# Kernel optimization log

Measured on AMD Instinct MI355X. Metric: run time of the kernel, lower is better.

Reference implementation:

```python
import jax, jax.numpy as jnp
import numpy as np

NUM_HEADS = 4
NUM_GROUPS = 32
EPS = 1e-5


def setup_inputs() -> dict:
    key = jax.random.key(0)
    ks = jax.random.split(key, 5)
    c = 256
    x = jax.random.normal(ks[0], (2, c, 64, 64), dtype=jnp.float32)
    gn_w = jnp.ones((c,), dtype=jnp.float32)
    gn_b = jnp.zeros((c,), dtype=jnp.float32)
    qkv_w = jax.random.normal(ks[1], (3 * c, c), dtype=jnp.float32) * 0.02
    qkv_b = jax.random.normal(ks[2], (3 * c,), dtype=jnp.float32) * 0.02
    proj_w = jax.random.normal(ks[3], (c, c), dtype=jnp.float32) * 0.02
    proj_b = jnp.zeros((c,), dtype=jnp.float32)
    return {"x": x, "gn_w": gn_w, "gn_b": gn_b, "qkv_w": qkv_w,
            "qkv_b": qkv_b, "proj_w": proj_w, "proj_b": proj_b}


def reference(x, gn_w, gn_b, qkv_w, qkv_b, proj_w, proj_b):
    b, c, H, W = x.shape
    T = H * W
    xf = x.reshape(b, c, T)

    # GroupNorm(32, c): stats over (channels-in-group, T)
    xg = xf.reshape(b, NUM_GROUPS, c // NUM_GROUPS, T)
    mu = jnp.mean(xg, axis=(2, 3), keepdims=True)
    var = jnp.var(xg, axis=(2, 3), keepdims=True)
    xn = ((xg - mu) * jax.lax.rsqrt(var + EPS)).reshape(b, c, T)
    xn = xn * gn_w[None, :, None] + gn_b[None, :, None]

    # 1x1 conv1d == channel matmul: [3c, c] @ [b, c, T]
    qkv = jnp.einsum('oc,bct->bot', qkv_w, xn) + qkv_b[None, :, None]

    nh = NUM_HEADS
    ch = c // nh
    # reshape exactly as torch: (b, 3c, T) -> (b*nh, 3c//nh, T), split along dim 1
    qkv = qkv.reshape(b * nh, 3 * ch, T)
    q, k, v = jnp.split(qkv, 3, axis=1)

    scale = 1.0 / ch ** 0.25
    w = jnp.einsum('bct,bcs->bts', q * scale, k * scale)  # [b*nh, T, T]
    w = jax.nn.softmax(w, axis=-1)
    h = jnp.einsum('bts,bcs->bct', w, v)  # [b*nh, ch, T]

    h = h.reshape(b, c, T)
    h = jnp.einsum('oc,bct->bot', proj_w, h) + proj_b[None, :, None]
    return (xf + h).reshape(b, c, H, W)
```

## Files before the change

### kernel.cpp

```cpp
#include <hip/hip_runtime.h>
#include <hip/hip_bf16.h>

typedef float  f32x4  __attribute__((ext_vector_type(4)));
typedef float  f32x16 __attribute__((ext_vector_type(16)));
typedef short  s16x8  __attribute__((ext_vector_type(8)));
typedef __bf16 b16x8  __attribute__((ext_vector_type(8)));
typedef unsigned int u32x4 __attribute__((ext_vector_type(4)));

#define DI static __device__ __forceinline__

constexpr int BATCH = 2;
constexpr int C     = 256;
constexpr int T     = 4096;
constexpr int NG    = 32;
constexpr int CPG   = 8;
constexpr int NH    = 4;
constexpr int CH    = 64;

constexpr size_t STATS_OFF = 0;
constexpr size_t QKVW_OFF  = 4096;
constexpr size_t PROJW_OFF = QKVW_OFF + 393216;
constexpr size_t XNT_OFF   = PROJW_OFF + 131072;
constexpr size_t Q_OFF     = XNT_OFF + 4194304;
constexpr size_t K_OFF     = Q_OFF + 4194304;
constexpr size_t V_OFF     = K_OFF + 4194304;
constexpr size_t H_OFF     = V_OFF + 4194304;

template <typename V>
DI auto mfma_try(V a, V b, f32x4 c, int)
    -> decltype(__builtin_amdgcn_mfma_f32_16x16x32_bf16(a, b, c, 0, 0, 0)) {
  return __builtin_amdgcn_mfma_f32_16x16x32_bf16(a, b, c, 0, 0, 0);
}
template <typename V>
DI f32x4 mfma_try(V a, V b, f32x4 c, long) {
  return __builtin_amdgcn_mfma_f32_16x16x32_bf16(
      __builtin_bit_cast(b16x8, a), __builtin_bit_cast(b16x8, b), c, 0, 0, 0);
}
DI f32x4 MFMA(s16x8 a, s16x8 b, f32x4 c) { return mfma_try(a, b, c, 0); }

template <typename V>
DI auto mfma32_try(V a, V b, f32x16 c, int)
    -> decltype(__builtin_amdgcn_mfma_f32_32x32x16_bf16(a, b, c, 0, 0, 0)) {
  return __builtin_amdgcn_mfma_f32_32x32x16_bf16(a, b, c, 0, 0, 0);
}
template <typename V>
DI f32x16 mfma32_try(V a, V b, f32x16 c, long) {
  return __builtin_amdgcn_mfma_f32_32x32x16_bf16(
      __builtin_bit_cast(b16x8, a), __builtin_bit_cast(b16x8, b), c, 0, 0, 0);
}
DI f32x16 MFMA32(s16x8 a, s16x8 b, f32x16 c) { return mfma32_try(a, b, c, 0); }

DI unsigned short f2b(float f) {
  return __builtin_bit_cast(unsigned short, __float2bfloat16(f));
}
DI s16x8 ld8(const unsigned short* p) { return *(const s16x8*)p; }

DI float exp2f_(float x) {
#if __has_builtin(__builtin_amdgcn_exp2f)
  return __builtin_amdgcn_exp2f(x);
#else
  return exp2f(x);
#endif
}

DI unsigned cvtpk(float lo, float hi) {
  unsigned r;
  asm("v_cvt_pk_bf16_f32 %0, %1, %2" : "=v"(r) : "v"(lo), "v"(hi));
  return r;
}

DI void swap32(unsigned& a, unsigned& b) {
#if __has_builtin(__builtin_amdgcn_permlane32_swap)
  auto r = __builtin_amdgcn_permlane32_swap((int)a, (int)b, false, false);
  a = (unsigned)r[0];
  b = (unsigned)r[1];
#else
  unsigned as = (unsigned)__shfl_xor((int)a, 32);
  unsigned bs = (unsigned)__shfl_xor((int)b, 32);
  if (threadIdx.x & 32) a = bs; else b = as;
#endif
}

DI void stage16(const void* g, void* l) {
  __builtin_amdgcn_global_load_lds((__attribute__((address_space(1))) const void*)g,
                                   (__attribute__((address_space(3))) void*)l, 16, 0, 0);
}

DI float vsum16(f32x16 v) {
  float p0 = (v[0] + v[1]) + (v[2] + v[3]);
  float p1 = (v[4] + v[5]) + (v[6] + v[7]);
  float p2 = (v[8] + v[9]) + (v[10] + v[11]);
  float p3 = (v[12] + v[13]) + (v[14] + v[15]);
  return (p0 + p1) + (p2 + p3);
}

constexpr float SC2 = 0.18033688011f;

__global__ __launch_bounds__(256) void k_prep(const float* __restrict__ x,
                                              float2* __restrict__ part,
                                              const float* __restrict__ qkvw,
                                              const float* __restrict__ projw,
                                              uint2* __restrict__ qwb,
                                              uint2* __restrict__ pwb) {
  int blk = blockIdx.x;
  if (blk < 256) {
    const float4* base = (const float4*)(x + (size_t)blk * 8192);
    float s = 0.f, ss = 0.f;
    for (int i = threadIdx.x; i < 2048; i += 256) {
      float4 v = base[i];
      s  += v.x + v.y + v.z + v.w;
      ss += v.x * v.x + v.y * v.y + v.z * v.z + v.w * v.w;
    }
#pragma unroll
    for (int off = 32; off > 0; off >>= 1) {
      s  += __shfl_down(s, off);
      ss += __shfl_down(ss, off);
    }
    __shared__ float sm[4], sm2[4];
    int wid = threadIdx.x >> 6;
    if ((threadIdx.x & 63) == 0) { sm[wid] = s; sm2[wid] = ss; }
    __syncthreads();
    if (threadIdx.x == 0)
      part[blk] = make_float2(sm[0] + sm[1] + sm[2] + sm[3], sm2[0] + sm2[1] + sm2[2] + sm2[3]);
  } else {
    int i = (blk - 256) * 256 + threadIdx.x;
    if (i < 3 * C * C / 4) {
      float4 v = ((const float4*)qkvw)[i];
      qwb[i] = make_uint2(cvtpk(v.x, v.y), cvtpk(v.z, v.w));
    }
    if (i < C * C / 4) {
      float4 v = ((const float4*)projw)[i];
      pwb[i] = make_uint2(cvtpk(v.x, v.y), cvtpk(v.z, v.w));
    }
  }
}

__global__ __launch_bounds__(256) void k_gnapply(const float* __restrict__ x,
                                                 const float2* __restrict__ part,
                                                 const float* __restrict__ gnw,
                                                 const float* __restrict__ gnb,
                                                 unsigned short* __restrict__ xnT) {
  __shared__ float tile[64][69];
  int b = blockIdx.z, c0 = blockIdx.y * 64, t0 = blockIdx.x * 64;
  int tid = threadIdx.x;
  int tl = tid & 63, cq = tid >> 6;
  const float inv = 1.f / (float)(CPG * T);
#pragma unroll
  for (int i = 0; i < 16; i++) {
    int c = c0 + cq + i * 4;
    int g4 = (b * NG + c / CPG) * 4;
    float2 p0 = part[g4], p1 = part[g4 + 1], p2 = part[g4 + 2], p3 = part[g4 + 3];
    float S = p0.x + p1.x + p2.x + p3.x;
    float SS = p0.y + p1.y + p2.y + p3.y;
    float mu = S * inv;
    float rsd = rsqrtf(SS * inv - mu * mu + 1e-5f);
    float v = x[((size_t)b * C + c) * T + t0 + tl];
    tile[cq + i * 4][tl] = (v - mu) * rsd * gnw[c] + gnb[c];
  }
  __syncthreads();
  int unit = tid & 7, tw = tid >> 3;
#pragma unroll
  for (int it = 0; it < 2; it++) {
    int t_l = tw + it * 32;
    float v[8];
#pragma unroll
    for (int k = 0; k < 8; k++) v[k] = tile[unit * 8 + k][t_l];
    u32x4 o = {cvtpk(v[0], v[1]), cvtpk(v[2], v[3]), cvtpk(v[4], v[5]), cvtpk(v[6], v[7])};
    *(u32x4*)(xnT + ((size_t)b * T + t0 + t_l) * C + c0 + unit * 8) = o;
  }
}

__global__ __launch_bounds__(512) void k_qkv(const unsigned short* __restrict__ wq,
                                             const float* __restrict__ bias,
                                             const unsigned short* __restrict__ xnT,
                                             unsigned short* __restrict__ qb,
                                             unsigned short* __restrict__ kb,
                                             unsigned short* __restrict__ vb) {
  int b = blockIdx.z;
  int o0 = blockIdx.y * 128;
  int t0 = blockIdx.x * 128;
  int tid = threadIdx.x, lane = tid & 63, wid = tid >> 6;
  int l31 = lane & 31, h = lane >> 5;
  int ow = (wid & 3) * 32;
  int th = (wid >> 2) * 64;
  const unsigned short* xp = xnT + (size_t)b * T * C;

  __shared__ __align__(16) char smem[131072];
  unsigned short* XL = (unsigned short*)smem;
  unsigned short* WL = (unsigned short*)(smem + 65536);

#pragma unroll
  for (int call = 0; call < 8; call++) {
    int row = call * 16 + wid * 2 + h;
    stage16(xp + (size_t)(t0 + row) * C + ((l31 ^ (row & 31)) * 8),
            smem + call * 8192 + wid * 1024);
  }
#pragma unroll
  for (int call = 0; call < 8; call++) {
    int row = call * 16 + wid * 2 + h;
    stage16(wq + (size_t)(o0 + row) * C + ((l31 ^ (row & 31)) * 8),
            smem + 65536 + call * 8192 + wid * 1024);
  }
  __syncthreads();

  f32x16 acc[2] = {};
  int ro = ow + l31;
  int rosw = ro & 31;
  int rt0 = th + l31, rt1 = th + 32 + l31;
  int rt0sw = rt0 & 31, rt1sw = rt1 & 31;
#pragma unroll
  for (int kc = 0; kc < C; kc += 16) {
    int u = (kc >> 3) + h;
    s16x8 a = ld8(WL + ro * 256 + ((u ^ rosw) * 8));
    s16x8 b0 = ld8(XL + rt0 * 256 + ((u ^ rt0sw) * 8));
    s16x8 b1 = ld8(XL + rt1 * 256 + ((u ^ rt1sw) * 8));
    acc[0] = MFMA32(a, b0, acc[0]);
    acc[1] = MFMA32(a, b1, acc[1]);
  }

  int mo = o0 + ow;
  int region = (mo >> 6) % 3;
  int hh = mo / 192;
  int bh = b * NH + hh;
  int rb = mo - hh * 192 - region * 64;
  float qsc = (region == 0) ? SC2 : 1.0f;
#pragma unroll
  for (int sub = 0; sub < 2; sub++) {
    int t = t0 + th + sub * 32 + l31;
#pragma unroll
    for (int rq = 0; rq < 4; rq++) {
      int obase = mo + 4 * h + 8 * rq;
      if (region < 2) {
        unsigned short pk[4];
#pragma unroll
        for (int j = 0; j < 4; j++)
          pk[j] = f2b((acc[sub][rq * 4 + j] + bias[obase + j]) * qsc);
        unsigned short* dst = (region == 0 ? qb : kb) + ((size_t)bh * T + t) * CH + rb + 4 * h + 8 * rq;
        *(ushort4*)dst = make_ushort4(pk[0], pk[1], pk[2], pk[3]);
      } else {
#pragma unroll
        for (int j = 0; j < 4; j++)
          vb[((size_t)bh * CH + rb + 4 * h + 8 * rq + j) * T + t] =
              f2b(acc[sub][rq * 4 + j] + bias[obase + j]);
      }
    }
  }
}

__global__ __launch_bounds__(512, 2) void k_attn6(const unsigned short* __restrict__ qb,
                                                  const unsigned short* __restrict__ kb,
                                                  const unsigned short* __restrict__ vb,
                                                  unsigned short* __restrict__ hb) {
  int bid = blockIdx.x;
  int lin = (bid & 7) * 32 + (bid >> 3);
  int qt = lin & 31;
  int bh = lin >> 5;
  int tid = threadIdx.x;
  int wid = tid >> 6, lane = tid & 63;
  int l31 = lane & 31, h = lane >> 5;
  int wq = wid & 1, g = wid >> 1;
  int qbase = qt * 128 + wq * 64;

  constexpr int SG = T / 4;
  constexpr int NT = SG / 64;

  const unsigned short* qp = qb + (size_t)bh * T * CH;
  const unsigned short* kp = kb + (size_t)bh * T * CH;
  const unsigned short* vp = vb + (size_t)bh * CH * T;
  unsigned short* hp = hb + (size_t)bh * T * CH;

  __shared__ __align__(16) char smem[131072];
  char* gbase = smem + g * 32768;

  s16x8 qfA[4], qfB[4];
#pragma unroll
  for (int kc = 0; kc < 4; kc++) {
    qfA[kc] = ld8(qp + (size_t)(qbase + l31) * CH + kc * 16 + h * 8);
    qfB[kc] = ld8(qp + (size_t)(qbase + 32 + l31) * CH + kc * 16 + h * 8);
  }

  f32x16 O0a = {}, O1a = {}, O0b = {}, O1b = {};
  float lA = 0.f, lB = 0.f;

  int srow = lane >> 3, su = lane & 7;
  const unsigned short* kS = kp + (size_t)(g * SG + srow) * CH + (su ^ srow) * 8;
  const unsigned short* vS = vp + (size_t)srow * T + g * SG + (su ^ srow) * 8;

#define STAGE(BUF, TT)                                                        \
  {                                                                           \
    char* slab_ = gbase + (BUF) * 16384;                                      \
    if (wq == 0) {                                                            \
      const unsigned short* s_ = kS + (size_t)(TT) * 64 * CH;                 \
      _Pragma("unroll") for (int j_ = 0; j_ < 8; j_++)                        \
          stage16(s_ + j_ * 8 * CH, slab_ + j_ * 1024);                       \
    } else {                                                                  \
      const unsigned short* s_ = vS + (size_t)(TT) * 64;                      \
      _Pragma("unroll") for (int j_ = 0; j_ < 8; j_++)                        \
          stage16(s_ + (size_t)j_ * 8 * T, slab_ + 8192 + j_ * 1024);         \
    }                                                                         \
  }

  int buf = 0;
  STAGE(0, 0);
  __syncthreads();

  int rsw = l31 & 7;
  int row0 = l31, row1 = 32 + l31;
  for (int t = 0; t < NT; ++t) {
    if (t + 1 < NT) STAGE(buf ^ 1, t + 1);
    const unsigned short* Kt = (const unsigned short*)(gbase + buf * 16384);
    const unsigned short* Vt = Kt + 4096;

    f32x16 S0a = {}, S1a = {}, S0b = {}, S1b = {};
    __builtin_amdgcn_s_setprio(1);
#pragma unroll
    for (int kc = 0; kc < 4; kc++) {
      s16x8 k0 = ld8(Kt + row0 * 64 + (((kc * 2 + h) ^ rsw) * 8));
      s16x8 k1 = ld8(Kt + row1 * 64 + (((kc * 2 + h) ^ rsw) * 8));
      S0a = MFMA32(k0, qfA[kc], S0a);
      S0b = MFMA32(k0, qfB[kc], S0b);
      S1a = MFMA32(k1, qfA[kc], S1a);
      S1b = MFMA32(k1, qfB[kc], S1b);
    }
    __builtin_amdgcn_s_setprio(0);

#pragma unroll
    for (int j = 0; j < 16; j++) {
      S0a[j] = exp2f_(S0a[j]);
      S1a[j] = exp2f_(S1a[j]);
      S0b[j] = exp2f_(S0b[j]);
      S1b[j] = exp2f_(S1b[j]);
    }
    lA += vsum16(S0a) + vsum16(S1a);
    lB += vsum16(S0b) + vsum16(S1b);

    __builtin_amdgcn_s_setprio(1);
#pragma unroll
    for (int sch = 0; sch < 4; sch++) {
      const f32x16& Sa = (sch < 2) ? S0a : S1a;
      const f32x16& Sb = (sch < 2) ? S0b : S1b;
      int o = (sch & 1) * 8;
      unsigned a0 = cvtpk(Sa[o + 0], Sa[o + 1]), a1 = cvtpk(Sa[o + 2], Sa[o + 3]);
      unsigned a2 = cvtpk(Sa[o + 4], Sa[o + 5]), a3 = cvtpk(Sa[o + 6], Sa[o + 7]);
      swap32(a0, a2); swap32(a1, a3);
      u32x4 pA = {a0, a1, a2, a3};
      unsigned b0 = cvtpk(Sb[o + 0], Sb[o + 1]), b1 = cvtpk(Sb[o + 2], Sb[o + 3]);
      unsigned b2 = cvtpk(Sb[o + 4], Sb[o + 5]), b3 = cvtpk(Sb[o + 6], Sb[o + 7]);
      swap32(b0, b2); swap32(b1, b3);
      u32x4 pB = {b0, b1, b2, b3};
      s16x8 pfA = __builtin_bit_cast(s16x8, pA);
      s16x8 pfB = __builtin_bit_cast(s16x8, pB);
      s16x8 v0 = ld8(Vt + row0 * 64 + (((sch * 2 + h) ^ rsw) * 8));
      s16x8 v1 = ld8(Vt + row1 * 64 + (((sch * 2 + h) ^ rsw) * 8));
      O0a = MFMA32(v0, pfA, O0a);
      O1a = MFMA32(v1, pfA, O1a);
      O0b = MFMA32(v0, pfB, O0b);
      O1b = MFMA32(v1, pfB, O1b);
    }
    __builtin_amdgcn_s_setprio(0);
    __syncthreads();
    buf ^= 1;
  }

  lA += __shfl_xor(lA, 32);
  lB += __shfl_xor(lB, 32);
  constexpr int SLOT = 67;
  float* cmbA = (float*)smem;
  float* cmbB = cmbA + 256 * SLOT;
  if (g >= 2) {
    float* dst = cmbA + (((g - 2) * 2 + wq) * 64 + lane) * SLOT;
#pragma unroll
    for (int j = 0; j < 16; j++) {
      dst[j] = O0a[j]; dst[16 + j] = O1a[j];
      dst[32 + j] = O0b[j]; dst[48 + j] = O1b[j];
    }
    dst[64] = lA; dst[65] = lB;
  }
  __syncthreads();
  if (g < 2) {
    const float* src = cmbA + ((g * 2 + wq) * 64 + lane) * SLOT;
#pragma unroll
    for (int j = 0; j < 16; j++) {
      O0a[j] += src[j];
      O1a[j] += src[16 + j];
      O0b[j] += src[32 + j];
      O1b[j] += src[48 + j];
    }
    lA += src[64]; lB += src[65];
  }
  __syncthreads();
  if (g == 1) {
    float* dst = cmbB + (wq * 64 + lane) * SLOT;
#pragma unroll
    for (int j = 0; j < 16; j++) {
      dst[j] = O0a[j]; dst[16 + j] = O1a[j];
      dst[32 + j] = O0b[j]; dst[48 + j] = O1b[j];
    }
    dst[64] = lA; dst[65] = lB;
  }
  __syncthreads();
  if (g == 0) {
    const float* src = cmbB + (wq * 64 + lane) * SLOT;
    float invA = 1.f / (lA + src[64]);
    float invB = 1.f / (lB + src[65]);
    int qA = qbase + l31, qB = qbase + 32 + l31;
#pragma unroll
    for (int j = 0; j < 16; j += 2) {
      int ch = (j & 3) + 8 * (j >> 2) + 4 * h;
      float y0 = (O0a[j] + src[j]) * invA;
      float y1 = (O0a[j + 1] + src[j + 1]) * invA;
      *(unsigned*)(hp + (size_t)qA * CH + ch) = cvtpk(y0, y1);
      float z0 = (O1a[j] + src[16 + j]) * invA;
      float z1 = (O1a[j + 1] + src[16 + j + 1]) * invA;
      *(unsigned*)(hp + (size_t)qA * CH + 32 + ch) = cvtpk(z0, z1);
      float u0 = (O0b[j] + src[32 + j]) * invB;
      float u1 = (O0b[j + 1] + src[32 + j + 1]) * invB;
      *(unsigned*)(hp + (size_t)qB * CH + ch) = cvtpk(u0, u1);
      float w0 = (O1b[j] + src[48 + j]) * invB;
      float w1 = (O1b[j + 1] + src[48 + j + 1]) * invB;
      *(unsigned*)(hp + (size_t)qB * CH + 32 + ch) = cvtpk(w0, w1);
    }
  }
}

__global__ __launch_bounds__(256) void k_proj(const unsigned short* __restrict__ wp,
                                              const float* __restrict__ bias,
                                              const unsigned short* __restrict__ hb,
                                              const float* __restrict__ x,
                                              float* __restrict__ out) {
  int b = blockIdx.z, o0 = blockIdx.y * 128, t0 = blockIdx.x * 64;
  int tid = threadIdx.x, lane = tid & 63, wid = tid >> 6;
  int l31 = lane & 31, h = lane >> 5;
  int ow = wid * 32;

  __shared__ __align__(16) char smem[98304];
  unsigned short* WL = (unsigned short*)smem;
  unsigned short* HL = (unsigned short*)(smem + 65536);

#pragma unroll
  for (int call = 0; call < 16; call++) {
    int rbase = call * 8 + wid * 2;
    int row = rbase + h;
    stage16(wp + (size_t)(o0 + row) * C + ((l31 ^ (row & 31)) * 8),
            smem + rbase * 512);
  }
#pragma unroll
  for (int call = 0; call < 8; call++) {
    int rbase = call * 8 + wid * 2;
    int row = rbase + h;
    int du = l31 ^ (row & 31);
    stage16(hb + ((size_t)(b * NH + (du >> 3)) * T + t0 + row) * CH + (du & 7) * 8,
            smem + 65536 + rbase * 512);
  }
  __syncthreads();

  f32x16 acc0 = {}, acc1 = {};
  int ro = ow + l31, rosw = ro & 31;
  int rt0 = l31, rt1 = 32 + l31;
  int rt0sw = rt0 & 31, rt1sw = rt1 & 31;
#pragma unroll
  for (int kc = 0; kc < C; kc += 16) {
    int u = (kc >> 3) + h;
    s16x8 a  = ld8(WL + ro * 256 + ((u ^ rosw) * 8));
    s16x8 b0 = ld8(HL + rt0 * 256 + ((u ^ rt0sw) * 8));
    s16x8 b1 = ld8(HL + rt1 * 256 + ((u ^ rt1sw) * 8));
    acc0 = MFMA32(a, b0, acc0);
    acc1 = MFMA32(a, b1, acc1);
  }

#pragma unroll
  for (int sub = 0; sub < 2; sub++) {
    const f32x16& acc = sub ? acc1 : acc0;
    int t = t0 + sub * 32 + l31;
#pragma unroll
    for (int reg = 0; reg < 16; reg++) {
      int o = o0 + ow + (reg & 3) + 8 * (reg >> 2) + 4 * h;
      size_t idx = ((size_t)b * C + o) * T + t;
      out[idx] = x[idx] + bias[o] + acc[reg];
    }
  }
}

extern "C" void kernel_launch(void* const* d_in, const int* in_sizes, int n_in,
                              void* d_out, int out_size, void* d_ws, size_t ws_size,
                              hipStream_t stream) {
  const float* x     = (const float*)d_in[0];
  const float* gnw   = (const float*)d_in[1];
  const float* gnb   = (const float*)d_in[2];
  const float* qkvw  = (const float*)d_in[3];
  const float* qkvb  = (const float*)d_in[4];
  const float* projw = (const float*)d_in[5];
  const float* projb = (const float*)d_in[6];
  float* out = (float*)d_out;
  char* ws = (char*)d_ws;

  float2* part          = (float2*)(ws + STATS_OFF);
  unsigned short* qw_b  = (unsigned short*)(ws + QKVW_OFF);
  unsigned short* pw_b  = (unsigned short*)(ws + PROJW_OFF);
  unsigned short* xnT   = (unsigned short*)(ws + XNT_OFF);
  unsigned short* qbuf  = (unsigned short*)(ws + Q_OFF);
  unsigned short* kbuf  = (unsigned short*)(ws + K_OFF);
  unsigned short* vbuf  = (unsigned short*)(ws + V_OFF);
  unsigned short* hbuf  = (unsigned short*)(ws + H_OFF);

  k_prep   <<<dim3(448), dim3(256), 0, stream>>>(x, part, qkvw, projw, (uint2*)qw_b, (uint2*)pw_b);
  k_gnapply<<<dim3(T / 64, C / 64, BATCH), dim3(256), 0, stream>>>(x, part, gnw, gnb, xnT);
  k_qkv    <<<dim3(T / 128, (3 * C) / 128, BATCH), dim3(512), 0, stream>>>(qw_b, qkvb, xnT, qbuf, kbuf, vbuf);
  k_attn6  <<<dim3(256), dim3(512), 0, stream>>>(qbuf, kbuf, vbuf, hbuf);
  k_proj   <<<dim3(T / 64, C / 128, BATCH), dim3(256), 0, stream>>>(pw_b, projb, hbuf, x, out);
}
```

Measured before the change: 74.18 us.

## Split attention work across 16 waves with 32 queries per wave

Each 1024-thread attention block now runs 16 waves in place of 8. Each wave owns 32 query rows instead of 64, and K/V staging is split across four waves per group. The aim is more waves per CU to hide LDS and exp latency, and fewer accumulator registers per wave. The costs are twice as many LDS reads of the K/V tiles per query, and a strict __launch_bounds__(1024, 4) that may squeeze the register budget and cause spills.

```diff
diff --git a/kernel.cpp b/kernel.cpp
--- a/kernel.cpp
+++ b/kernel.cpp
@@ -247,10 +247,10 @@
   }
 }
 
-__global__ __launch_bounds__(512, 2) void k_attn6(const unsigned short* __restrict__ qb,
-                                                  const unsigned short* __restrict__ kb,
-                                                  const unsigned short* __restrict__ vb,
-                                                  unsigned short* __restrict__ hb) {
+__global__ __launch_bounds__(1024, 4) void k_attn8(const unsigned short* __restrict__ qb,
+                                                   const unsigned short* __restrict__ kb,
+                                                   const unsigned short* __restrict__ vb,
+                                                   unsigned short* __restrict__ hb) {
   int bid = blockIdx.x;
   int lin = (bid & 7) * 32 + (bid >> 3);
   int qt = lin & 31;
@@ -258,8 +258,8 @@
   int tid = threadIdx.x;
   int wid = tid >> 6, lane = tid & 63;
   int l31 = lane & 31, h = lane >> 5;
-  int wq = wid & 1, g = wid >> 1;
-  int qbase = qt * 128 + wq * 64;
+  int wq = wid & 3, g = wid >> 2;
+  int qbase = qt * 128 + wq * 32;
 
   constexpr int SG = T / 4;
   constexpr int NT = SG / 64;
@@ -272,15 +272,13 @@
   __shared__ __align__(16) char smem[131072];
   char* gbase = smem + g * 32768;
 
-  s16x8 qfA[4], qfB[4];
-#pragma unroll
-  for (int kc = 0; kc < 4; kc++) {
-    qfA[kc] = ld8(qp + (size_t)(qbase + l31) * CH + kc * 16 + h * 8);
-    qfB[kc] = ld8(qp + (size_t)(qbase + 32 + l31) * CH + kc * 16 + h * 8);
-  }
-
-  f32x16 O0a = {}, O1a = {}, O0b = {}, O1b = {};
-  float lA = 0.f, lB = 0.f;
+  s16x8 qf[4];
+#pragma unroll
+  for (int kc = 0; kc < 4; kc++)
+    qf[kc] = ld8(qp + (size_t)(qbase + l31) * CH + kc * 16 + h * 8);
+
+  f32x16 O0 = {}, O1 = {};
+  float lsum = 0.f;
 
   int srow = lane >> 3, su = lane & 7;
   const unsigned short* kS = kp + (size_t)(g * SG + srow) * CH + (su ^ srow) * 8;
@@ -289,14 +287,18 @@
 #define STAGE(BUF, TT)                                                        \
   {                                                                           \
     char* slab_ = gbase + (BUF) * 16384;                                      \
-    if (wq == 0) {                                                            \
+    if (wq < 2) {                                                             \
       const unsigned short* s_ = kS + (size_t)(TT) * 64 * CH;                 \
-      _Pragma("unroll") for (int j_ = 0; j_ < 8; j_++)                        \
-          stage16(s_ + j_ * 8 * CH, slab_ + j_ * 1024);                       \
+      _Pragma("unroll") for (int i_ = 0; i_ < 4; i_++) {                      \
+        int j_ = wq * 4 + i_;                                                 \
+        stage16(s_ + j_ * 8 * CH, slab_ + j_ * 1024);                         \
+      }                                                                       \
     } else {                                                                  \
       const unsigned short* s_ = vS + (size_t)(TT) * 64;                      \
-      _Pragma("unroll") for (int j_ = 0; j_ < 8; j_++)                        \
-          stage16(s_ + (size_t)j_ * 8 * T, slab_ + 8192 + j_ * 1024);         \
+      _Pragma("unroll") for (int i_ = 0; i_ < 4; i_++) {                      \
+        int j_ = (wq - 2) * 4 + i_;                                           \
+        stage16(s_ + (size_t)j_ * 8 * T, slab_ + 8192 + j_ * 1024);           \
+      }                                                                       \
     }                                                                         \
   }
 
@@ -311,114 +313,85 @@
     const unsigned short* Kt = (const unsigned short*)(gbase + buf * 16384);
     const unsigned short* Vt = Kt + 4096;
 
-    f32x16 S0a = {}, S1a = {}, S0b = {}, S1b = {};
+    f32x16 S0 = {}, S1 = {};
     __builtin_amdgcn_s_setprio(1);
 #pragma unroll
     for (int kc = 0; kc < 4; kc++) {
       s16x8 k0 = ld8(Kt + row0 * 64 + (((kc * 2 + h) ^ rsw) * 8));
       s16x8 k1 = ld8(Kt + row1 * 64 + (((kc * 2 + h) ^ rsw) * 8));
-      S0a = MFMA32(k0, qfA[kc], S0a);
-      S0b = MFMA32(k0, qfB[kc], S0b);
-      S1a = MFMA32(k1, qfA[kc], S1a);
-      S1b = MFMA32(k1, qfB[kc], S1b);
+      S0 = MFMA32(k0, qf[kc], S0);
+      S1 = MFMA32(k1, qf[kc], S1);
     }
     __builtin_amdgcn_s_setprio(0);
 
 #pragma unroll
     for (int j = 0; j < 16; j++) {
-      S0a[j] = exp2f_(S0a[j]);
-      S1a[j] = exp2f_(S1a[j]);
-      S0b[j] = exp2f_(S0b[j]);
-      S1b[j] = exp2f_(S1b[j]);
-    }
-    lA += vsum16(S0a) + vsum16(S1a);
-    lB += vsum16(S0b) + vsum16(S1b);
+      S0[j] = exp2f_(S0[j]);
+      S1[j] = exp2f_(S1[j]);
+    }
+    lsum += vsum16(S0) + vsum16(S1);
 
     __builtin_amdgcn_s_setprio(1);
 #pragma unroll
     for (int sch = 0; sch < 4; sch++) {
-      const f32x16& Sa = (sch < 2) ? S0a : S1a;
-      const f32x16& Sb = (sch < 2) ? S0b : S1b;
+      const f32x16& Sa = (sch < 2) ? S0 : S1;
       int o = (sch & 1) * 8;
       unsigned a0 = cvtpk(Sa[o + 0], Sa[o + 1]), a1 = cvtpk(Sa[o + 2], Sa[o + 3]);
       unsigned a2 = cvtpk(Sa[o + 4], Sa[o + 5]), a3 = cvtpk(Sa[o + 6], Sa[o + 7]);
       swap32(a0, a2); swap32(a1, a3);
       u32x4 pA = {a0, a1, a2, a3};
-      unsigned b0 = cvtpk(Sb[o + 0], Sb[o + 1]), b1 = cvtpk(Sb[o + 2], Sb[o + 3]);
-      unsigned b2 = cvtpk(Sb[o + 4], Sb[o + 5]), b3 = cvtpk(Sb[o + 6], Sb[o + 7]);
-      swap32(b0, b2); swap32(b1, b3);
-      u32x4 pB = {b0, b1, b2, b3};
-      s16x8 pfA = __builtin_bit_cast(s16x8, pA);
-      s16x8 pfB = __builtin_bit_cast(s16x8, pB);
+      s16x8 pf = __builtin_bit_cast(s16x8, pA);
       s16x8 v0 = ld8(Vt + row0 * 64 + (((sch * 2 + h) ^ rsw) * 8));
       s16x8 v1 = ld8(Vt + row1 * 64 + (((sch * 2 + h) ^ rsw) * 8));
-      O0a = MFMA32(v0, pfA, O0a);
-      O1a = MFMA32(v1, pfA, O1a);
-      O0b = MFMA32(v0, pfB, O0b);
-      O1b = MFMA32(v1, pfB, O1b);
+      O0 = MFMA32(v0, pf, O0);
+      O1 = MFMA32(v1, pf, O1);
     }
     __builtin_amdgcn_s_setprio(0);
     __syncthreads();
     buf ^= 1;
   }
 
-  lA += __shfl_xor(lA, 32);
-  lB += __shfl_xor(lB, 32);
-  constexpr int SLOT = 67;
+  lsum += __shfl_xor(lsum, 32);
+  constexpr int SLOT = 35;
   float* cmbA = (float*)smem;
-  float* cmbB = cmbA + 256 * SLOT;
+  float* cmbB = cmbA + 512 * SLOT;
   if (g >= 2) {
-    float* dst = cmbA + (((g - 2) * 2 + wq) * 64 + lane) * SLOT;
+    float* dst = cmbA + (((g - 2) * 4 + wq) * 64 + lane) * SLOT;
+#pragma unroll
+    for (int j = 0; j < 16; j++) { dst[j] = O0[j]; dst[16 + j] = O1[j]; }
+    dst[32] = lsum;
+  }
+  __syncthreads();
+  if (g < 2) {
+    const float* src = cmbA + ((g * 4 + wq) * 64 + lane) * SLOT;
 #pragma unroll
     for (int j = 0; j < 16; j++) {
-      dst[j] = O0a[j]; dst[16 + j] = O1a[j];
-      dst[32 + j] = O0b[j]; dst[48 + j] = O1b[j];
-    }
-    dst[64] = lA; dst[65] = lB;
-  }
-  __syncthreads();
-  if (g < 2) {
-    const float* src = cmbA + ((g * 2 + wq) * 64 + lane) * SLOT;
-#pragma unroll
-    for (int j = 0; j < 16; j++) {
-      O0a[j] += src[j];
-      O1a[j] += src[16 + j];
-      O0b[j] += src[32 + j];
-      O1b[j] += src[48 + j];
-    }
-    lA += src[64]; lB += src[65];
+      O0[j] += src[j];
+      O1[j] += src[16 + j];
+    }
+    lsum += src[32];
   }
   __syncthreads();
   if (g == 1) {
     float* dst = cmbB + (wq * 64 + lane) * SLOT;
 #pragma unroll
-    for (int j = 0; j < 16; j++) {
-      dst[j] = O0a[j]; dst[16 + j] = O1a[j];
-      dst[32 + j] = O0b[j]; dst[48 + j] = O1b[j];
-    }
-    dst[64] = lA; dst[65] = lB;
+    for (int j = 0; j < 16; j++) { dst[j] = O0[j]; dst[16 + j] = O1[j]; }
+    dst[32] = lsum;
   }
   __syncthreads();
   if (g == 0) {
     const float* src = cmbB + (wq * 64 + lane) * SLOT;
-    float invA = 1.f / (lA + src[64]);
-    float invB = 1.f / (lB + src[65]);
-    int qA = qbase + l31, qB = qbase + 32 + l31;
+    float inv = 1.f / (lsum + src[32]);
+    int q = qbase + l31;
 #pragma unroll
     for (int j = 0; j < 16; j += 2) {
       int ch = (j & 3) + 8 * (j >> 2) + 4 * h;
-      float y0 = (O0a[j] + src[j]) * invA;
-      float y1 = (O0a[j + 1] + src[j + 1]) * invA;
-      *(unsigned*)(hp + (size_t)qA * CH + ch) = cvtpk(y0, y1);
-      float z0 = (O1a[j] + src[16 + j]) * invA;
-      float z1 = (O1a[j + 1] + src[16 + j + 1]) * invA;
-      *(unsigned*)(hp + (size_t)qA * CH + 32 + ch) = cvtpk(z0, z1);
-      float u0 = (O0b[j] + src[32 + j]) * invB;
-      float u1 = (O0b[j + 1] + src[32 + j + 1]) * invB;
-      *(unsigned*)(hp + (size_t)qB * CH + ch) = cvtpk(u0, u1);
-      float w0 = (O1b[j] + src[48 + j]) * invB;
-      float w1 = (O1b[j + 1] + src[48 + j + 1]) * invB;
-      *(unsigned*)(hp + (size_t)qB * CH + 32 + ch) = cvtpk(w0, w1);
+      float y0 = (O0[j] + src[j]) * inv;
+      float y1 = (O0[j + 1] + src[j + 1]) * inv;
+      *(unsigned*)(hp + (size_t)q * CH + ch) = cvtpk(y0, y1);
+      float z0 = (O1[j] + src[16 + j]) * inv;
+      float z1 = (O1[j + 1] + src[16 + j + 1]) * inv;
+      *(unsigned*)(hp + (size_t)q * CH + 32 + ch) = cvtpk(z0, z1);
     }
   }
 }
@@ -506,6 +479,6 @@
   k_prep   <<<dim3(448), dim3(256), 0, stream>>>(x, part, qkvw, projw, (uint2*)qw_b, (uint2*)pw_b);
   k_gnapply<<<dim3(T / 64, C / 64, BATCH), dim3(256), 0, stream>>>(x, part, gnw, gnb, xnT);
   k_qkv    <<<dim3(T / 128, (3 * C) / 128, BATCH), dim3(512), 0, stream>>>(qw_b, qkvb, xnT, qbuf, kbuf, vbuf);
-  k_attn6  <<<dim3(256), dim3(512), 0, stream>>>(qbuf, kbuf, vbuf, hbuf);
+  k_attn8  <<<dim3(256), dim3(1024), 0, stream>>>(qbuf, kbuf, vbuf, hbuf);
   k_proj   <<<dim3(T / 64, C / 128, BATCH), dim3(256), 0, stream>>>(pw_b, projb, hbuf, x, out);
 }
```

Result: no change. 73.36 us, median of 3 (-1.1%).
